# Kernel optimization log

Hardware: AMD Instinct MI355X
Metric: run time of the kernel (lower is better)

Reference implementation:

```python
import jax, jax.numpy as jnp
import numpy as np
from jax import lax

NH = 8  # heads


def _ln(x, g, b):
    m = x.mean(-1, keepdims=True)
    v = ((x - m) ** 2).mean(-1, keepdims=True)
    return (x - m) * lax.rsqrt(v + 1e-5) * g + b


def _pos_idx(n):
    # torch: linspace(n-1,0,n)[:,None] + linspace(0,n-1,n)[None,:], flattened long
    r = np.linspace(n - 1, 0, n).reshape(n, 1)
    c = np.linspace(0, n - 1, n).reshape(1, n)
    return jnp.asarray((r + c).reshape(-1).astype(np.int32))


def _mha(q_in, k_in, v_in, in_w, in_b, out_w, out_b, pos_enc=None, pos_idx=None, attn_mask=None):
    # MultiheadAttentionRelative: q/k/v proj + relative pos-encoding gather terms
    w, bsz, e = q_in.shape
    hd = e // NH
    scale = hd ** -0.5
    q = (q_in @ in_w[:e].T + in_b[:e]) * scale
    k = k_in @ in_w[e:2 * e].T + in_b[e:2 * e]
    v = v_in @ in_w[2 * e:].T + in_b[2 * e:]
    q = q.reshape(w, bsz, NH, hd)
    k = k.reshape(w, bsz, NH, hd)
    v = v.reshape(w, bsz, NH, hd)
    attn = jnp.einsum('wnec,vnec->newv', q, k)  # [N,E,W,W']
    if pos_enc is not None:
        pe = pos_enc[pos_idx].reshape(w, w, e)  # [2W-1,C] -> [W,W',C] gather
        q_r = ((pe @ in_w[:e].T + in_b[:e]) * scale).reshape(w, w, NH, hd)
        k_r = (pe @ in_w[e:2 * e].T + in_b[e:2 * e]).reshape(w, w, NH, hd)
        attn = attn + jnp.einsum('wnec,wvec->newv', q, k_r) + jnp.einsum('vnec,wvec->newv', k, q_r)
    if attn_mask is not None:
        attn = attn + attn_mask[None, None]
    raw = attn
    p = jax.nn.softmax(attn, axis=-1)
    v_o = jnp.einsum('newv,vnec->wnec', p, v).reshape(w, bsz, e)
    return v_o @ out_w.T + out_b, raw.sum(axis=1)


def _interp_lin(x, out_size):
    # torch F.interpolate(mode='linear', align_corners=False) along last axis
    L_in = x.shape[-1]
    if L_in == out_size:
        return x
    coords = jnp.clip((jnp.arange(out_size, dtype=jnp.float32) + 0.5) * (L_in / out_size) - 0.5, 0.0, L_in - 1.0)
    lo = jnp.floor(coords).astype(jnp.int32)
    hi = jnp.minimum(lo + 1, L_in - 1)
    frac = coords - lo.astype(jnp.float32)
    return x[..., lo] * (1.0 - frac) + x[..., hi] * frac


def _conv(x, w, b, pad):
    y = lax.conv_general_dilated(x, w, (1, 1), pad, dimension_numbers=('NCHW', 'OIHW', 'NCHW'))
    return y + b[None, :, None, None]


def _self_layer(feat, feat1, pos, pidx, pos1, pidx1, posy, pidxy, posy1, pidxy1, p):
    iw, ib, ow, ob, n1g, n1b, n2g, n2b = p
    f2 = _ln(feat, n1g, n1b)
    f4 = _ln(feat1, n2g, n2b)
    w_, h2, c = f2.shape
    w1_, h4, c1 = f4.shape
    # row<->col switch: [W,2HN,C] -> [HN,2W,C]
    f2y = jnp.transpose(f2.reshape(w_, 2, h2 // 2, c), (2, 1, 0, 3)).reshape(h2 // 2, 2 * w_, c)
    f4y = jnp.transpose(f4.reshape(w1_, 2, h4 // 2, c1), (2, 1, 0, 3)).reshape(h4 // 2, 2 * w1_, c1)
    f2y, _ = _mha(f2y, f2y, f2y, iw[1], ib[1], ow[1], ob[1], posy, pidxy)
    f2 = jnp.transpose(f2y.reshape(h2 // 2, 2, w_, c), (2, 1, 0, 3)).reshape(w_, h2, c)
    f4y, _ = _mha(f4y, f4y, f4y, iw[3], ib[3], ow[3], ob[3], posy1, pidxy1)
    f4 = jnp.transpose(f4y.reshape(h4 // 2, 2, w1_, c1), (2, 1, 0, 3)).reshape(w1_, h4, c1)
    f2, _ = _mha(f2, f2, f2, iw[0], ib[0], ow[0], ob[0], pos, pidx)
    f4, _ = _mha(f4, f4, f4, iw[2], ib[2], ow[2], ob[2], pos1, pidx1)
    return feat + f2, feat1 + f4


def _cross_layer(fl, fr, fl1, fr1, pos, pidx, pos1, pidx1, p, last):
    iw, ib, ow, ob, n1g, n1b, n2g, n2b, mw1, mb1, mw2, mb2 = p
    fl2 = _ln(fl, n1g, n1b)
    fr2 = _ln(fr, n1g, n1b)
    fl4 = _ln(fl1, n2g, n2b)
    fr4 = _ln(fr1, n2g, n2b)
    up_r, _ = _mha(fr2, fl2, fl2, iw[0], ib[0], ow[0], ob[0], jnp.flip(pos, 0), pidx)
    up_r1, _ = _mha(fr4, fl4, fl4, iw[1], ib[1], ow[1], ob[1], jnp.flip(pos1, 0), pidx1)
    fr = fr + up_r
    fr1n = fr1 + up_r1
    if last:
        w = fl2.shape[0]
        w1 = fl4.shape[0]
        m = jnp.where(jnp.triu(jnp.ones((w, w), jnp.float32), 1) == 1.0, -jnp.inf, 0.0)
        m1 = jnp.where(jnp.triu(jnp.ones((w1, w1), jnp.float32), 1) == 1.0, -jnp.inf, 0.0)
    else:
        m = None
        m1 = None
    fr2n = _ln(fr, n1g, n1b)
    up_l, raw = _mha(fl2, fr2n, fr2n, iw[0], ib[0], ow[0], ob[0], pos, pidx, m)
    fr4n = _ln(fr1n, n2g, n2b)
    up_l1, _ = _mha(fl4, fr4n, fr4n, iw[1], ib[1], ow[1], ob[1], pos1, pidx1, m1)
    fl = fl + up_l
    fl1n = fl1 + up_l1
    feat = jnp.concatenate([fl, fr], 1)        # [W,2HN,C]
    feat_n = jnp.concatenate([fl1n, fr1n], 1)  # [W1,2HN,C]
    x = jnp.transpose(feat_n, (2, 1, 0))       # [C,2HN,W1]
    x = _interp_lin(x, feat.shape[0])          # [C,2HN,W]
    feat_n = jnp.transpose(x, (2, 1, 0))
    feat_n = jnp.concatenate([feat_n, feat], 2)  # [W,2HN,2C]
    x = jnp.transpose(feat_n, (2, 1, 0))[None]   # [1,2C,2HN,W]
    x = _conv(x, mw1, mb1, 'VALID')
    x = _conv(x, mw2, mb2, ((1, 1), (1, 1)))
    out = jnp.transpose(x[0], (2, 1, 0))         # [W,2HN,C]
    return out, raw


def reference(feat_left, feat_right, feat_left1, feat_right1, pos_enc, pos_enc1, pos_enc_y, pos_enc_y1,
              sa_in_w, sa_in_b, sa_out_w, sa_out_b, sa_n1_g, sa_n1_b, sa_n2_g, sa_n2_b,
              ca_in_w, ca_in_b, ca_out_w, ca_out_b, ca_n1_g, ca_n1_b, ca_n2_g, ca_n2_b,
              merge_w1, merge_b1, merge_w2, merge_b2):
    bs, c, h, w = feat_left.shape
    w1 = feat_left1.shape[3]
    hn = h * bs

    def flat(x):
        return jnp.transpose(x, (3, 2, 0, 1)).reshape(x.shape[3], -1, c)  # [W,HN,C]

    fl, fr = flat(feat_left), flat(feat_right)
    fl1, fr1 = flat(feat_left1), flat(feat_right1)
    pidx = _pos_idx(w)
    pidx1 = _pos_idx(w1)
    pidxy = _pos_idx(hn)
    pidxy1 = _pos_idx(hn)
    feat = jnp.concatenate([fl, fr], 1)    # [W,2HN,C]
    feat1 = jnp.concatenate([fl1, fr1], 1)  # [W1,2HN,C]
    L = sa_in_w.shape[0]
    raw = None
    for i in range(L):
        sp = (sa_in_w[i], sa_in_b[i], sa_out_w[i], sa_out_b[i], sa_n1_g[i], sa_n1_b[i], sa_n2_g[i], sa_n2_b[i])
        feat, feat1 = _self_layer(feat, feat1, pos_enc, pidx, pos_enc1, pidx1, pos_enc_y, pidxy, pos_enc_y1, pidxy1, sp)
        cp = (ca_in_w[i], ca_in_b[i], ca_out_w[i], ca_out_b[i], ca_n1_g[i], ca_n1_b[i], ca_n2_g[i], ca_n2_b[i],
              merge_w1[i], merge_b1[i], merge_w2[i], merge_b2[i])
        feat, raw = _cross_layer(feat[:, :hn], feat[:, hn:], feat1[:, :hn], feat1[:, hn:],
                                 pos_enc, pidx, pos_enc1, pidx1, cp, i == L - 1)
    attn_weight = jnp.transpose(raw.reshape(h, bs, w, w), (1, 0, 2, 3))  # [N,H,W,W]
    return attn_weight


def setup_inputs() -> dict:
    key = jax.random.key(0)
    ks = iter(jax.random.split(key, 40))
    N, C, H, W, W1, Lyr = 1, 128, 64, 128, 64, 6
    s = 0.05
    d = {}
    d['feat_left'] = jax.random.normal(next(ks), (N, C, H, W), jnp.float32)
    d['feat_right'] = jax.random.normal(next(ks), (N, C, H, W), jnp.float32)
    d['feat_left1'] = jax.random.normal(next(ks), (N, C, H, W1), jnp.float32)
    d['feat_right1'] = jax.random.normal(next(ks), (N, C, H, W1), jnp.float32)
    d['pos_enc'] = jax.random.normal(next(ks), (2 * W - 1, C), jnp.float32) * 0.1
    d['pos_enc1'] = jax.random.normal(next(ks), (2 * W1 - 1, C), jnp.float32) * 0.1
    d['pos_enc_y'] = jax.random.normal(next(ks), (2 * H - 1, C), jnp.float32) * 0.1
    d['pos_enc_y1'] = jax.random.normal(next(ks), (2 * H - 1, C), jnp.float32) * 0.1
    d['sa_in_w'] = jax.random.normal(next(ks), (Lyr, 4, 3 * C, C), jnp.float32) * s
    d['sa_in_b'] = jnp.zeros((Lyr, 4, 3 * C), jnp.float32)
    d['sa_out_w'] = jax.random.normal(next(ks), (Lyr, 4, C, C), jnp.float32) * s
    d['sa_out_b'] = jnp.zeros((Lyr, 4, C), jnp.float32)
    d['sa_n1_g'] = jnp.ones((Lyr, C), jnp.float32)
    d['sa_n1_b'] = jnp.zeros((Lyr, C), jnp.float32)
    d['sa_n2_g'] = jnp.ones((Lyr, C), jnp.float32)
    d['sa_n2_b'] = jnp.zeros((Lyr, C), jnp.float32)
    d['ca_in_w'] = jax.random.normal(next(ks), (Lyr, 2, 3 * C, C), jnp.float32) * s
    d['ca_in_b'] = jnp.zeros((Lyr, 2, 3 * C), jnp.float32)
    d['ca_out_w'] = jax.random.normal(next(ks), (Lyr, 2, C, C), jnp.float32) * s
    d['ca_out_b'] = jnp.zeros((Lyr, 2, C), jnp.float32)
    d['ca_n1_g'] = jnp.ones((Lyr, C), jnp.float32)
    d['ca_n1_b'] = jnp.zeros((Lyr, C), jnp.float32)
    d['ca_n2_g'] = jnp.ones((Lyr, C), jnp.float32)
    d['ca_n2_b'] = jnp.zeros((Lyr, C), jnp.float32)
    d['merge_w1'] = jax.random.normal(next(ks), (Lyr, 128, 256, 1, 1), jnp.float32) * s
    d['merge_b1'] = jnp.zeros((Lyr, 128), jnp.float32)
    d['merge_w2'] = jax.random.normal(next(ks), (Lyr, 128, 128, 3, 3), jnp.float32) * s
    d['merge_b2'] = jnp.zeros((Lyr, 128), jnp.float32)
    return d
```

## Files before the change

### kernel.cpp

```cpp
#include <hip/hip_runtime.h>
#include <hip/hip_bf16.h>
#include <math.h>


typedef __attribute__((ext_vector_type(8))) short bf16x8;
typedef __attribute__((ext_vector_type(4))) float f32x4;
typedef __hip_bfloat16 bf16;

__device__ __forceinline__ float b2f(unsigned short u) {
  return __uint_as_float((unsigned)u << 16);
}
__device__ __forceinline__ short f2bs(float x) {
  bf16 h = __float2bfloat16(x);
  short s;
  __builtin_memcpy(&s, &h, 2);
  return s;
}
__device__ __forceinline__ int ymap(int t, int D0, int D1) {
  return (t % D0) * (2 * D1) + ((t / D0) & 1) * D1 + t / (2 * D0);
}


__global__ void k_build_feat(const float* __restrict__ L, const float* __restrict__ R,
                             float* __restrict__ feat, int W) {
  int t = blockIdx.x;
  int c = threadIdx.x;
  int b = t & 127;
  int w = t >> 7;
  const float* src = (b < 64) ? L : R;
  int h = b & 63;
  feat[(size_t)t * 128 + c] = src[((size_t)c * 64 + h) * W + w];
}

struct FDesc { const float* s; bf16* d; int n; };
struct FArgs { FDesc d[9]; int cum[10]; int nprob; };
__global__ void k_f2b_multi(FArgs fa) {
  int bid = blockIdx.x;
  int p = 0;
  while (p + 1 < fa.nprob && bid >= fa.cum[p + 1]) ++p;
  const FDesc d = fa.d[p];
  int i = (bid - fa.cum[p]) * 1024 + threadIdx.x * 4;
  if (i + 3 < d.n) {
    float4 x = *(const float4*)(d.s + i);
    d.d[i + 0] = __float2bfloat16(x.x);
    d.d[i + 1] = __float2bfloat16(x.y);
    d.d[i + 2] = __float2bfloat16(x.z);
    d.d[i + 3] = __float2bfloat16(x.w);
  } else {
    for (int z = 0; z < 4 && i + z < d.n; ++z) d.d[i + z] = __float2bfloat16(d.s[i + z]);
  }
}

__global__ void k_wfullb(const float* __restrict__ w2, bf16* __restrict__ wf) {
  int bid = blockIdx.x;
  int l = bid >> 7, co = bid & 127;
  int ci = threadIdx.x;
  const float* src = w2 + (size_t)l * 128 * 128 * 9;
  bf16* dst = wf + (size_t)l * 128 * 1152;
#pragma unroll
  for (int ky = 0; ky < 3; ky++)
#pragma unroll
    for (int kx = 0; kx < 3; kx++)
      dst[(size_t)co * 1152 + (kx * 3 + ky) * 128 + ci] =
          __float2bfloat16(src[((size_t)(co * 128 + ci) * 3 + ky) * 3 + kx]);
}

__global__ void k_zero_guard(bf16* p0, bf16* p1) {
  int t = threadIdx.x;
  p0[255 * 256 + t] = __float2bfloat16(0.0f);
  p1[127 * 256 + t] = __float2bfloat16(0.0f);
}

struct WCArgs { const bf16* iw[12]; const bf16* ow[12]; bf16* out[12]; };
__global__ __launch_bounds__(256) void k_wcomb(WCArgs a) {
  __shared__ bf16 sOw[128 * 128];
  int p = blockIdx.x / 6, rc = blockIdx.x % 6;
  const bf16* iw = a.iw[p];
  const bf16* ow = a.ow[p];
  for (int i = threadIdx.x; i < 128 * 16; i += 256)
    ((bf16x8*)sOw)[i] = ((const bf16x8*)ow)[i];
  __syncthreads();
  int row = rc * 64 + (threadIdx.x >> 2);
  int seg = (threadIdx.x & 3) * 32;
  float acc[32];
#pragma unroll
  for (int c = 0; c < 32; ++c) acc[c] = 0.f;
  for (int t = 0; t < 128; ++t) {
    float av = b2f((unsigned short)iw[row * 128 + t]);
#pragma unroll
    for (int c = 0; c < 32; ++c)
      acc[c] = fmaf(av, b2f((unsigned short)sOw[t * 128 + seg + c]), acc[c]);
  }
  bf16* o = a.out[p] + (size_t)row * 128 + seg;
  for (int c = 0; c < 32; ++c) o[c] = __float2bfloat16(acc[c]);
}

struct BCArgs { const float* iwf[12]; const float* obf[12]; const float* ibf[12]; float* out[12]; };
__global__ void k_bcomb(BCArgs a) {
  int p = blockIdx.x, j = threadIdx.x;
  const float* iw = a.iwf[p] + (size_t)j * 128;
  const float* ob = a.obf[p];
  float acc = a.ibf[p][j];
  for (int t = 0; t < 128; ++t) acc = fmaf(iw[t], ob[t], acc);
  a.out[p][j] = acc;
}

__global__ void k_rawcomb4(const float* __restrict__ A, const float* __restrict__ B2,
                           const float* __restrict__ C3, const float* __restrict__ D4,
                           bf16* __restrict__ out) {
  int i = blockIdx.x * 256 + threadIdx.x;
  int v = i & 127, w = (i >> 7) & 127;
  float rv = (v > w) ? 0.0f : (A[i] + B2[i] + C3[i] + D4[i]);
  out[i] = __float2bfloat16(rv);
}


struct LDesc { const float* src; bf16* dst; const float* g; const float* be;
               int ntok, Bout, PBin, offIn; };
struct LArgs { LDesc d[4]; int cum[5]; int nprob; };

__global__ __launch_bounds__(256) void k_ln_multi(LArgs la) {
  int bid = blockIdx.x;
  int p = 0;
  while (p + 1 < la.nprob && bid >= la.cum[p + 1]) ++p;
  const LDesc d = la.d[p];
  int t = (bid - la.cum[p]) * 4 + (threadIdx.x >> 6);
  int lane = threadIdx.x & 63;
  if (t >= d.ntok) return;
  int w = t / d.Bout, b = t - w * d.Bout;
  const float* row = d.src + (size_t)(w * d.PBin + d.offIn + b) * 128;
  float x0 = row[lane], x1 = row[lane + 64];
  float s = x0 + x1;
#pragma unroll
  for (int o = 32; o; o >>= 1) s += __shfl_xor(s, o, 64);
  float m = s * (1.0f / 128.0f);
  float d0 = x0 - m, d1 = x1 - m;
  float v = d0 * d0 + d1 * d1;
#pragma unroll
  for (int o = 32; o; o >>= 1) v += __shfl_xor(v, o, 64);
  float r = 1.0f / sqrtf(v * (1.0f / 128.0f) + 1e-5f);
  bf16* orow = d.dst + (size_t)t * 128;
  orow[lane]      = __float2bfloat16(d0 * r * d.g[lane]      + d.be[lane]);
  orow[lane + 64] = __float2bfloat16(d1 * r * d.g[lane + 64] + d.be[lane + 64]);
}


struct GDesc {
  const bf16* A; const float* Af0; const float* Af1;
  const bf16* W; const float* bias;
  bf16* Cb; float* Cf; const float* resid;
  int M, N, K, lda, scaleN;
  int imode, iD0, iD1;
  int omode, oD0, oD1, ooff;
};
struct GArgs { GDesc d[6]; int cum[7]; int nprob; };

__global__ __launch_bounds__(256) void k_gemm_multi(GArgs ga) {
  __shared__ bf16x8 sA[64 * 4];
  __shared__ bf16x8 sB[64 * 4];
  int bid = blockIdx.x;
  int p = 0;
  while (p + 1 < ga.nprob && bid >= ga.cum[p + 1]) ++p;
  const GDesc d = ga.d[p];
  int local = bid - ga.cum[p];
  int tilesx = d.N >> 6;
  int ty = local / tilesx, tx = local - ty * tilesx;
  const int m0 = ty << 6, n0 = tx << 6;
  const int tid = threadIdx.x;
  const int lane = tid & 63;
  const int wave = tid >> 6;
  const int wm = wave >> 1, wn = wave & 1;
  const int fr = lane & 15;
  const int kc = lane >> 4;
  f32x4 acc[2][2];
#pragma unroll
  for (int f = 0; f < 2; f++)
#pragma unroll
    for (int g = 0; g < 2; g++) acc[f][g] = (f32x4){0.f, 0.f, 0.f, 0.f};

  for (int k0 = 0; k0 < d.K; k0 += 32) {
    {
      int row = tid >> 2, ch = tid & 3;
      int m = m0 + row;
      bf16x8 val = (bf16x8){0, 0, 0, 0, 0, 0, 0, 0};
      if (d.imode == 0) {
        if (m < d.M) val = *(const bf16x8*)(d.A + (size_t)m * d.lda + k0 + ch * 8);
      } else if (d.imode == 1) {
        if (m < d.M) {
          int ar = ymap(m, d.iD0, d.iD1);
          val = *(const bf16x8*)(d.A + (size_t)ar * d.lda + k0 + ch * 8);
        }
      } else if (d.imode == 2) {
        int kblk = k0 >> 7;
        int kx = kblk / 3, ky = kblk - kx * 3;
        int arow = m + (kx - 1) * 128;
        int y = (m & 127) + (ky - 1);
        if (arow >= 0 && arow < d.M && y >= 0 && y < 128)
          val = *(const bf16x8*)(d.A + (size_t)arow * d.lda + (k0 & 127) + ch * 8);
      } else {
        int kk = k0 + ch * 8;
        int w = m >> 7, y = m & 127;
        if (kk < 128) {
          float xo = fminf(fmaxf(w * 0.5f - 0.25f, 0.0f), 63.0f);
          int lo = (int)xo;
          int hi = (lo + 1 < 63) ? lo + 1 : 63;
          float f = xo - (float)lo;
          const float* a0 = d.Af0 + ((size_t)lo * 128 + y) * 128 + kk;
          const float* a1 = d.Af0 + ((size_t)hi * 128 + y) * 128 + kk;
#pragma unroll
          for (int z = 0; z < 8; ++z) val[z] = f2bs(a0[z] * (1.0f - f) + a1[z] * f);
        } else {
          const float* a0 = d.Af1 + (size_t)m * 128 + (kk - 128);
#pragma unroll
          for (int z = 0; z < 8; ++z) val[z] = f2bs(a0[z]);
        }
      }
      sA[row * 4 + (ch ^ ((row >> 2) & 3))] = val;
      bf16x8 bval = *(const bf16x8*)(d.W + (size_t)(n0 + row) * d.K + k0 + ch * 8);
      sB[row * 4 + (ch ^ ((row >> 2) & 3))] = bval;
    }
    __syncthreads();
    bf16x8 af[2], bg[2];
#pragma unroll
    for (int f = 0; f < 2; ++f) {
      int row = wm * 32 + f * 16 + fr;
      af[f] = sA[row * 4 + (kc ^ ((row >> 2) & 3))];
    }
#pragma unroll
    for (int g = 0; g < 2; ++g) {
      int row = wn * 32 + g * 16 + fr;
      bg[g] = sB[row * 4 + (kc ^ ((row >> 2) & 3))];
    }
#pragma unroll
    for (int f = 0; f < 2; ++f)
#pragma unroll
      for (int g = 0; g < 2; ++g)
        acc[f][g] = __builtin_amdgcn_mfma_f32_16x16x32_bf16(af[f], bg[g], acc[f][g], 0, 0, 0);
    __syncthreads();
  }
  const int r4 = (lane >> 4) << 2;
  const int ocol = lane & 15;
#pragma unroll
  for (int f = 0; f < 2; ++f) {
#pragma unroll
    for (int g = 0; g < 2; ++g) {
      int n = n0 + wn * 32 + g * 16 + ocol;
      float bv = d.bias ? d.bias[n] : 0.0f;
      bool sc = (n < d.scaleN);
#pragma unroll
      for (int i = 0; i < 4; ++i) {
        int m = m0 + wm * 32 + f * 16 + r4 + i;
        if (m < d.M) {
          int row;
          if (d.omode == 0) row = (m / d.oD0) * d.oD1 + d.ooff + (m % d.oD0);
          else row = ymap(m, d.oD0, d.oD1);
          size_t idx = (size_t)row * d.N + n;
          float val = acc[f][g][i] + bv;
          if (sc) val *= 0.25f;
          if (d.resid) val += d.resid[idx];
          if (d.Cb) d.Cb[idx] = __float2bfloat16(val);
          else d.Cf[idx] = val;
        }
      }
    }
  }
}


struct ADesc {
  const bf16* Q; const bf16* K; const bf16* V;
  const bf16* PPb; bf16* O;
  float* raw0; float* raw1; float* raw2; float* raw3;
  int ldQ, ldK, ldV, Wlen, B, sflip, useMask;
};
struct AArgs { ADesc d[2]; int cum[3]; int nprob; };

template<int WLEN, int SGN>
__device__ __forceinline__ void attn_core(const ADesc& d, int b, int st, int h,
                                          int tid, bf16* Vt, bf16* Pl, bf16* T2l,
                                          bf16* Ost) {
  constexpr int NT = WLEN / 16;
  constexpr int R = WLEN - 1;
  const f32x4 z4 = (f32x4){0.f, 0.f, 0.f, 0.f};
  const bf16x8 zb = (bf16x8){0, 0, 0, 0, 0, 0, 0, 0};

  {
    int q = tid & (WLEN / 2 - 1);
    int cc = tid >> ((WLEN == 128) ? 6 : 5);
    constexpr int CH = (WLEN == 128) ? 16 : 8;
    int cb = cc * CH;
    const bf16* v0p = d.V + ((size_t)(2 * q) * d.B + b) * d.ldV + h * 64 + cb;
    const bf16* v1p = d.V + ((size_t)(2 * q + 1) * d.B + b) * d.ldV + h * 64 + cb;
#pragma unroll
    for (int j = 0; j < CH; j += 8) {
      bf16x8 a = *(const bf16x8*)(v0p + j);
      bf16x8 bb = *(const bf16x8*)(v1p + j);
#pragma unroll
      for (int z = 0; z < 8; ++z) {
        unsigned pk = (unsigned)(unsigned short)a[z] |
                      ((unsigned)(unsigned short)bb[z] << 16);
        *(unsigned*)(Vt + (size_t)(cb + j + z) * 136 + 2 * q) = pk;
      }
    }
  }
  __syncthreads();

  const int wave = tid >> 6, l = tid & 63;
  const int lm = l & 15, lg = l >> 4;
  const bool zlane = (lg >= 2);
  bf16* Pw  = Pl + wave * (16 * 136);
  bf16* T2w = T2l + wave * (16 * 20);
  int p0[4], src[4], hi[4], tsel[4];
  bool csel[4];
#pragma unroll
  for (int i = 0; i < 4; ++i) {
    p0[i] = SGN * (lm - 4 * lg - i) + 15;
    src[i] = (l & 48) | (p0[i] & 15);
    hi[i] = p0[i] & 16;
    if (SGN == 1) {
      int t0 = lm + 15 - 4 * lg - i;
      csel[i] = (t0 < 16);
      tsel[i] = csel[i] ? t0 : t0 - 16;
    } else {
      int t0 = lm - 15 + 4 * lg + i;
      csel[i] = (t0 >= 0);
      tsel[i] = csel[i] ? t0 : t0 + 16;
    }
  }

  const int w0 = st * 16;
  const int chb = h * 64 + wave * 16 + lg * 8;

  bf16x8 qf = zb;
  if (!zlane) qf = *(const bf16x8*)(d.Q + ((size_t)(w0 + lm) * d.B + b) * d.ldQ + chb);

  const int U0 = (SGN == 1) ? (R - w0 - 15) : (R + w0 - WLEN + 1);
  const int Ub0 = (SGN == 1) ? (R - w0 - 15) : (R - (WLEN - 16) + w0 - 15);
  const bf16* t1p = d.PPb + (size_t)(U0 + lm) * 256 + 128 + chb;
  const bf16* t2p = d.PPb + (size_t)(Ub0 + lm) * 256 + chb;
  const int v0i = ((SGN == 1) ? 0 : (WLEN - 16)) + lm;
  const bf16* kp = d.K + ((size_t)v0i * d.B + b) * d.ldK + chb;
  const ptrdiff_t kstep = (ptrdiff_t)SGN * 16 * d.B * d.ldK;

  f32x4 t1a;
  {
    bf16x8 z = zb;
    if (!zlane) z = *(const bf16x8*)t1p;
    t1p += 16 * 256;
    t1a = __builtin_amdgcn_mfma_f32_16x16x32_bf16(qf, z, z4, 0, 0, 0);
  }
  int v = v0i;
#pragma unroll
  for (int j = 0; j < NT; ++j) {
    f32x4 t1b;
    {
      bf16x8 z = zb;
      if (!zlane) z = *(const bf16x8*)t1p;
      t1p += 16 * 256;
      t1b = __builtin_amdgcn_mfma_f32_16x16x32_bf16(qf, z, z4, 0, 0, 0);
    }
    bf16x8 kf = zb;
    if (!zlane) kf = *(const bf16x8*)kp;
    kp += kstep;
    f32x4 s4 = __builtin_amdgcn_mfma_f32_16x16x32_bf16(qf, kf, z4, 0, 0, 0);
    bf16x8 zA = zb, zB = zb;
    if (!zlane) {
      zA = *(const bf16x8*)t2p;
      zB = *(const bf16x8*)(t2p + 16 * 256);
    }
    t2p += 16 * 256;
    f32x4 t2A = __builtin_amdgcn_mfma_f32_16x16x32_bf16(zA, kf, z4, 0, 0, 0);
    f32x4 t2B = __builtin_amdgcn_mfma_f32_16x16x32_bf16(zB, kf, z4, 0, 0, 0);
#pragma unroll
    for (int i = 0; i < 4; ++i)
      T2w[lm * 20 + tsel[i]] = f2bs(csel[i] ? t2A[i] : t2B[i]);
    ushort4 t2u = *(const ushort4*)(T2w + lm * 20 + 4 * lg);
    unsigned short t2a[4] = {t2u.x, t2u.y, t2u.z, t2u.w};
#pragma unroll
    for (int i = 0; i < 4; ++i) {
      float va = __shfl(t1a[i], src[i], 64);
      float vb = __shfl(t1b[i], src[i], 64);
      float s = s4[i] + (hi[i] ? vb : va) + b2f(t2a[i]);
      Pw[(4 * lg + i) * 136 + v] = f2bs(__expf(s));
    }
    t1a = t1b;
    v += SGN * 16;
  }
  const bf16x8 ones = (bf16x8){0x3F80, 0x3F80, 0x3F80, 0x3F80,
                               0x3F80, 0x3F80, 0x3F80, 0x3F80};
  f32x4 oa = z4, rsm = z4;
#pragma unroll
  for (int vc = 0; vc < NT / 2; ++vc) {
    bf16x8 pf = *(const bf16x8*)(Pw + lm * 136 + vc * 32 + lg * 8);
    bf16x8 vf = *(const bf16x8*)(Vt + (size_t)(wave * 16 + lm) * 136 + vc * 32 + lg * 8);
    oa = __builtin_amdgcn_mfma_f32_16x16x32_bf16(pf, vf, oa, 0, 0, 0);
    rsm = __builtin_amdgcn_mfma_f32_16x16x32_bf16(pf, ones, rsm, 0, 0, 0);
  }
#pragma unroll
  for (int i = 0; i < 4; ++i)
    Ost[(4 * lg + i) * 80 + wave * 16 + lm] = f2bs(oa[i] / rsm[i]);
  __syncthreads();
  if (tid < 128) {
    int row = tid >> 3, ch8 = (tid & 7) * 8;
    bf16x8 vv = *(const bf16x8*)(Ost + row * 80 + ch8);
    *(bf16x8*)(d.O + ((size_t)(w0 + row) * d.B + b) * 128 + h * 64 + ch8) = vv;
  }
}

__global__ __launch_bounds__(256, 4) void k_attn_mfma(AArgs aa) {
  __shared__ bf16 Vt[64 * 136];
  __shared__ bf16 Pl[4 * 16 * 136];
  __shared__ bf16 T2l[4 * 16 * 20];
  __shared__ bf16 Ost[16 * 80];
  int bid = blockIdx.x;
  int p = 0;
  while (p + 1 < aa.nprob && bid >= aa.cum[p + 1]) ++p;
  const ADesc d = aa.d[p];
  int local = bid - aa.cum[p];
  int b = local % d.B;
  int rest = local / d.B;
  int ns = d.Wlen >> 4;
  int st = rest % ns, h = rest / ns;
  int tid = threadIdx.x;
  if (d.Wlen == 128) {
    if (d.sflip == 1) attn_core<128, 1>(d, b, st, h, tid, Vt, Pl, T2l, Ost);
    else attn_core<128, -1>(d, b, st, h, tid, Vt, Pl, T2l, Ost);
  } else {
    if (d.sflip == 1) attn_core<64, 1>(d, b, st, h, tid, Vt, Pl, T2l, Ost);
    else attn_core<64, -1>(d, b, st, h, tid, Vt, Pl, T2l, Ost);
  }
}

__global__ __launch_bounds__(256, 2) void k_attn_raw(ADesc d) {
  __shared__ bf16 T2l[4 * 16 * 20];
  constexpr int NT = 8;
  constexpr int R = 127;
  const f32x4 z4 = (f32x4){0.f, 0.f, 0.f, 0.f};
  const bf16x8 zb = (bf16x8){0, 0, 0, 0, 0, 0, 0, 0};
  int bid = blockIdx.x;
  int b = bid % d.B, st = bid / d.B;
  int tid = threadIdx.x;
  const int wave = tid >> 6, l = tid & 63;
  const int lm = l & 15, lg = l >> 4;
  const bool zlane = (lg >= 2);
  bf16* T2w = T2l + wave * (16 * 20);
  int p0[4];
#pragma unroll
  for (int i = 0; i < 4; ++i) p0[i] = (lm - 4 * lg - i) + 15;
  const int w0 = st * 16;
  f32x4 raw[NT];
#pragma unroll
  for (int vt = 0; vt < NT; ++vt) raw[vt] = z4;

  for (int hh = 0; hh < 2; ++hh) {
    const int e = wave * 2 + hh;
    const int chb = e * 16 + lg * 8;
    bf16x8 qf = zb;
    if (!zlane) qf = *(const bf16x8*)(d.Q + ((size_t)(w0 + lm) * d.B + b) * d.ldQ + chb);
    const int U0 = R - w0 - 15;
    f32x4 t1a;
    {
      int u = min(max(U0 + lm, 0), 2 * R);
      bf16x8 z = zb;
      if (!zlane) z = *(const bf16x8*)(d.PPb + (size_t)u * 256 + 128 + chb);
      t1a = __builtin_amdgcn_mfma_f32_16x16x32_bf16(qf, z, z4, 0, 0, 0);
    }
#pragma unroll
    for (int j = 0; j < NT; ++j) {
      const int vt = j;
      const int v = vt * 16 + lm;
      f32x4 t1b;
      {
        int u = min(max(U0 + (j + 1) * 16 + lm, 0), 2 * R);
        bf16x8 z = zb;
        if (!zlane) z = *(const bf16x8*)(d.PPb + (size_t)u * 256 + 128 + chb);
        t1b = __builtin_amdgcn_mfma_f32_16x16x32_bf16(qf, z, z4, 0, 0, 0);
      }
      bf16x8 kf = zb;
      if (!zlane) kf = *(const bf16x8*)(d.K + ((size_t)v * d.B + b) * d.ldK + chb);
      f32x4 s4 = __builtin_amdgcn_mfma_f32_16x16x32_bf16(qf, kf, z4, 0, 0, 0);
      const int Ub = R + vt * 16 - w0 - 15;
#pragma unroll
      for (int u2 = 0; u2 < 2; ++u2) {
        int ua = min(max(Ub + u2 * 16 + lm, 0), 2 * R);
        bf16x8 z = zb;
        if (!zlane) z = *(const bf16x8*)(d.PPb + (size_t)ua * 256 + chb);
        f32x4 t2 = __builtin_amdgcn_mfma_f32_16x16x32_bf16(z, kf, z4, 0, 0, 0);
#pragma unroll
        for (int i = 0; i < 4; ++i) {
          int u = Ub + u2 * 16 + 4 * lg + i;
          int t = R + v - u - w0;
          if (t >= 0 && t < 16) T2w[lm * 20 + t] = f2bs(t2[i]);
        }
      }
      ushort4 t2u = *(const ushort4*)(T2w + lm * 20 + 4 * lg);
      unsigned short t2a[4] = {t2u.x, t2u.y, t2u.z, t2u.w};
#pragma unroll
      for (int i = 0; i < 4; ++i) {
        int src = (l & 48) | (p0[i] & 15);
        float va = __shfl(t1a[i], src, 64);
        float vb = __shfl(t1b[i], src, 64);
        float s = s4[i] + ((p0[i] & 16) ? vb : va) + b2f(t2a[i]);
        if (v > (w0 + 4 * lg + i)) s = -INFINITY;
        raw[vt][i] += s;
      }
      t1a = t1b;
    }
  }
  float* rp = (wave == 0) ? d.raw0 : (wave == 1) ? d.raw1 : (wave == 2) ? d.raw2 : d.raw3;
#pragma unroll
  for (int vt = 0; vt < NT; ++vt)
#pragma unroll
    for (int i = 0; i < 4; ++i)
      rp[((size_t)b * 128 + (w0 + 4 * lg + i)) * 128 + vt * 16 + lm] = raw[vt][i];
}


extern "C" void kernel_launch(void* const* d_in, const int* in_sizes, int n_in,
                              void* d_out, int out_size, void* d_ws, size_t ws_size,
                              hipStream_t stream) {
  (void)in_sizes; (void)n_in; (void)out_size; (void)ws_size;
  const float* FLt  = (const float*)d_in[0];
  const float* FRt  = (const float*)d_in[1];
  const float* FL1t = (const float*)d_in[2];
  const float* FR1t = (const float*)d_in[3];
  const float* PE   = (const float*)d_in[4];
  const float* PE1  = (const float*)d_in[5];
  const float* PEY  = (const float*)d_in[6];
  const float* PEY1 = (const float*)d_in[7];
  const float* SA_IW = (const float*)d_in[8];
  const float* SA_IB = (const float*)d_in[9];
  const float* SA_OW = (const float*)d_in[10];
  const float* SA_OB = (const float*)d_in[11];
  const float* SA_N1G = (const float*)d_in[12];
  const float* SA_N1B = (const float*)d_in[13];
  const float* SA_N2G = (const float*)d_in[14];
  const float* SA_N2B = (const float*)d_in[15];
  const float* CA_IW = (const float*)d_in[16];
  const float* CA_IB = (const float*)d_in[17];
  const float* CA_OW = (const float*)d_in[18];
  const float* CA_OB = (const float*)d_in[19];
  const float* CA_N1G = (const float*)d_in[20];
  const float* CA_N1B = (const float*)d_in[21];
  const float* CA_N2G = (const float*)d_in[22];
  const float* CA_N2B = (const float*)d_in[23];
  const float* MW1 = (const float*)d_in[24];
  const float* MB1 = (const float*)d_in[25];
  const float* MW2 = (const float*)d_in[26];
  const float* MB2 = (const float*)d_in[27];

  float* ws = (float*)d_ws;
  float* FEAT  = ws;
  float* FEAT1 = ws + 2097152;
  float* FN2   = ws + 3145728;
  bf16* PP0b   = (bf16*)(ws + 4194304);
  bf16* PP1b   = (bf16*)(ws + 4259840);
  float* B2f   = ws + 4276224;
  bf16* hb = (bf16*)(ws + 4292608);
  bf16* QKV   = hb;
  bf16* QKV1  = hb + 6291456;
  bf16* Xb    = hb + 9437184;
  bf16* XBb   = hb + 11534336;
  bf16* Ob    = hb + 12582912;
  bf16* Ob1   = hb + 14680064;
  bf16* PEb   = hb + 15728640;
  bf16* PE1b  = hb + 15761408;
  bf16* PEYb  = hb + 15777792;
  bf16* PEY1b = hb + 15794176;
  bf16* SAIWb = hb + 15810560;
  bf16* SAOWb = hb + 18169856;
  bf16* CAIWb = hb + 18563072;
  bf16* CAOWb = hb + 19742720;
  bf16* MW1b  = hb + 19939328;
  bf16* WFb   = hb + 20135936;
  bf16* W2b   = hb + 21020672;

  bf16* QR   = QKV + 3145728;
  bf16* FL4F = QKV + 4194304;
  bf16* QR1  = QKV + 5767168;
  bf16* KVq  = QKV1;
  bf16* KVq1 = QKV1 + 2097152;
  bf16* XR2  = Xb;
  bf16* XR21 = Xb + 1048576;

  GArgs ga; int ng = 0; int gb = 0;
  auto gadd = [&](GDesc gd) { ga.cum[ng] = gb; ga.d[ng] = gd;
                              gb += ((gd.M + 63) >> 6) * (gd.N >> 6); ++ng; };
  auto gflush = [&]() { ga.nprob = ng;
                        k_gemm_multi<<<gb, 256, 0, stream>>>(ga); ng = 0; gb = 0; };
  LArgs la; int nl = 0; int lb = 0;
  auto lnadd = [&](LDesc ld) { la.cum[nl] = lb; la.d[nl] = ld;
                               lb += (ld.ntok + 3) / 4; ++nl; };
  auto lnflush = [&]() { la.nprob = nl;
                         k_ln_multi<<<lb, 256, 0, stream>>>(la); nl = 0; lb = 0; };
  AArgs aa; int na = 0; int ab = 0;
  auto aadd = [&](ADesc ad) { aa.cum[na] = ab; aa.d[na] = ad;
                              ab += ad.B * (ad.Wlen >> 4) * 2; ++na; };
  auto aflush = [&]() { aa.nprob = na;
                        k_attn_mfma<<<ab, 256, 0, stream>>>(aa); na = 0; ab = 0; };

  auto G = [&](const bf16* A, const bf16* W, const float* bias,
               bf16* Cb, float* Cf, const float* resid,
               int M, int N, int K, int lda, int scaleN,
               int imode, int iD0, int iD1,
               int omode, int oD0, int oD1, int ooff,
               const float* Af0 = nullptr, const float* Af1 = nullptr) {
    GDesc gd; gd.A = A; gd.Af0 = Af0; gd.Af1 = Af1; gd.W = W; gd.bias = bias;
    gd.Cb = Cb; gd.Cf = Cf; gd.resid = resid;
    gd.M = M; gd.N = N; gd.K = K; gd.lda = lda; gd.scaleN = scaleN;
    gd.imode = imode; gd.iD0 = iD0; gd.iD1 = iD1;
    gd.omode = omode; gd.oD0 = oD0; gd.oD1 = oD1; gd.ooff = ooff;
    gadd(gd);
  };
  auto AT = [&](const bf16* Q, int ldQ, const bf16* K, int ldK, const bf16* V, int ldV,
                const bf16* PPb, int Wlen, int B, int sflip, bf16* O) {
    ADesc ad; ad.Q = Q; ad.K = K; ad.V = V; ad.PPb = PPb; ad.O = O;
    ad.raw0 = nullptr; ad.raw1 = nullptr; ad.raw2 = nullptr; ad.raw3 = nullptr;
    ad.ldQ = ldQ; ad.ldK = ldK; ad.ldV = ldV; ad.Wlen = Wlen; ad.B = B;
    ad.sflip = sflip; ad.useMask = 0;
    aadd(ad);
  };

  {
    FArgs fa; int nf = 0; int fb = 0;
    auto fadd = [&](const float* s, bf16* dd, int n) {
      fa.cum[nf] = fb; fa.d[nf] = FDesc{s, dd, n}; fb += (n + 1023) / 1024; ++nf; };
    fadd(SA_IW, SAIWb, 6 * 4 * 384 * 128);
    fadd(SA_OW, SAOWb, 6 * 4 * 128 * 128);
    fadd(CA_IW, CAIWb, 6 * 2 * 384 * 128);
    fadd(CA_OW, CAOWb, 6 * 2 * 128 * 128);
    fadd(MW1,   MW1b,  6 * 128 * 256);
    fadd(PE,    PEb,   255 * 128);
    fadd(PE1,   PE1b,  127 * 128);
    fadd(PEY,   PEYb,  127 * 128);
    fadd(PEY1,  PEY1b, 127 * 128);
    fa.nprob = nf;
    k_f2b_multi<<<fb, 256, 0, stream>>>(fa);
  }
  k_wfullb<<<768, 128, 0, stream>>>(MW2, WFb);
  k_zero_guard<<<1, 256, 0, stream>>>(PP0b, PP1b);
  {
    WCArgs wc; BCArgs bc;
    for (int l = 0; l < 6; ++l) {
      for (int s = 0; s < 2; ++s) {
        int p = l * 2 + s;
        int iwi = (s == 0) ? 0 : 2;
        int owi = (s == 0) ? 1 : 3;
        wc.iw[p]  = SAIWb + (size_t)l * 4 * 384 * 128 + (size_t)iwi * 384 * 128;
        wc.ow[p]  = SAOWb + (size_t)l * 4 * 128 * 128 + (size_t)owi * 128 * 128;
        wc.out[p] = W2b + (size_t)p * 384 * 128;
        bc.iwf[p] = SA_IW + (size_t)l * 4 * 384 * 128 + (size_t)iwi * 384 * 128;
        bc.obf[p] = SA_OB + (size_t)l * 4 * 128 + (size_t)owi * 128;
        bc.ibf[p] = SA_IB + (size_t)l * 4 * 384 + (size_t)iwi * 384;
        bc.out[p] = B2f + (size_t)p * 384;
      }
    }
    k_wcomb<<<72, 256, 0, stream>>>(wc);
    k_bcomb<<<12, 384, 0, stream>>>(bc);
  }
  k_build_feat<<<16384, 128, 0, stream>>>(FLt, FRt, FEAT, 128);
  k_build_feat<<<8192, 128, 0, stream>>>(FL1t, FR1t, FEAT1, 64);

  for (int l = 0; l < 6; ++l) {
    bool last = (l == 5);
    const bf16* iw  = SAIWb + (size_t)l * 4 * 384 * 128;
    const float* ib = SA_IB + (size_t)l * 4 * 384;
    const bf16* ow  = SAOWb + (size_t)l * 4 * 128 * 128;
    const float* ob = SA_OB + (size_t)l * 4 * 128;
    const bf16* ciw  = CAIWb + (size_t)l * 2 * 384 * 128;
    const float* cib = CA_IB + (size_t)l * 2 * 384;
    const bf16* cow  = CAOWb + (size_t)l * 2 * 128 * 128;
    const float* cob = CA_OB + (size_t)l * 2 * 128;
    const bf16* ciw1 = ciw + 384 * 128;
    const float* cib1 = cib + 384;
    const bf16* cow1 = cow + 128 * 128;
    const float* cob1 = cob + 128;
    const int IW = 384 * 128, OW = 128 * 128;

    lnadd(LDesc{FEAT, Xb, SA_N1G + l * 128, SA_N1B + l * 128, 16384, 128, 128, 0});
    if (!last) lnadd(LDesc{FEAT1, XBb, SA_N2G + l * 128, SA_N2B + l * 128, 8192, 128, 128, 0});
    lnflush();
    G(Xb, iw + IW, ib + 384, QKV, nullptr, nullptr, 16384, 384, 128, 128, 128, 1, 128, 64, 0, 1, 1, 0);
    if (!last) G(XBb, iw + 3 * IW, ib + 3 * 384, QKV1, nullptr, nullptr, 8192, 384, 128, 128, 128, 1, 64, 64, 0, 1, 1, 0);
    G(PEYb, iw + IW, ib + 384, PP0b, nullptr, nullptr, 127, 256, 128, 128, 128, 0, 0, 0, 0, 1, 1, 0);
    if (!last) G(PEY1b, iw + 3 * IW, ib + 3 * 384, PP1b, nullptr, nullptr, 127, 256, 128, 128, 128, 0, 0, 0, 0, 1, 1, 0);
    gflush();
    AT(QKV, 384, QKV + 128, 384, QKV + 256, 384, PP0b, 64, 256, 1, Ob);
    if (!last) AT(QKV1, 384, QKV1 + 128, 384, QKV1 + 256, 384, PP1b, 64, 128, 1, Ob1);
    aflush();
    G(Ob, W2b + (size_t)(l * 2) * 49152, B2f + (l * 2) * 384, QKV, nullptr, nullptr,
      16384, 384, 128, 128, 128, 1, 64, 128, 0, 1, 1, 0);
    if (!last) G(Ob1, W2b + (size_t)(l * 2 + 1) * 49152, B2f + (l * 2 + 1) * 384, QKV1,
                 nullptr, nullptr, 8192, 384, 128, 128, 128, 1, 64, 64, 0, 1, 1, 0);
    G(PEb, iw, ib, PP0b, nullptr, nullptr, 255, 256, 128, 128, 128, 0, 0, 0, 0, 1, 1, 0);
    if (!last) G(PE1b, iw + 2 * IW, ib + 2 * 384, PP1b, nullptr, nullptr, 127, 256, 128, 128, 128, 0, 0, 0, 0, 1, 1, 0);
    gflush();
    AT(QKV, 384, QKV + 128, 384, QKV + 256, 384, PP0b, 128, 128, 1, Ob);
    if (!last) AT(QKV1, 384, QKV1 + 128, 384, QKV1 + 256, 384, PP1b, 64, 128, 1, Ob1);
    aflush();
    G(Ob, ow, ob, nullptr, FEAT, FEAT, 16384, 128, 128, 128, 0, 0, 0, 0, 0, 1, 1, 0);
    if (!last) G(Ob1, ow + 2 * OW, ob + 2 * 128, nullptr, FEAT1, FEAT1, 8192, 128, 128, 128, 0, 0, 0, 0, 0, 1, 1, 0);
    gflush();

    lnadd(LDesc{FEAT, Xb, CA_N1G + l * 128, CA_N1B + l * 128, 8192, 64, 128, 0});
    lnadd(LDesc{FEAT, Xb + 1048576, CA_N1G + l * 128, CA_N1B + l * 128, 8192, 64, 128, 64});
    if (!last) {
      lnadd(LDesc{FEAT1, XBb, CA_N2G + l * 128, CA_N2B + l * 128, 4096, 64, 128, 0});
      lnadd(LDesc{FEAT1, XBb + 524288, CA_N2G + l * 128, CA_N2B + l * 128, 4096, 64, 128, 64});
    }
    lnflush();
    G(Xb, ciw, cib, QKV, nullptr, nullptr, 8192, 384, 128, 128, 128, 0, 0, 0, 0, 1, 1, 0);
    G(Xb + 1048576, ciw, cib, QR, nullptr, nullptr, 8192, 128, 128, 128, 128, 0, 0, 0, 0, 1, 1, 0);
    if (!last) {
      G(XBb, ciw1, cib1, FL4F, nullptr, nullptr, 4096, 384, 128, 128, 128, 0, 0, 0, 0, 1, 1, 0);
      G(XBb + 524288, ciw1, cib1, QR1, nullptr, nullptr, 4096, 128, 128, 128, 128, 0, 0, 0, 0, 1, 1, 0);
    }
    G(PEb, ciw, cib, PP0b, nullptr, nullptr, 255, 256, 128, 128, 128, 0, 0, 0, 0, 1, 1, 0);
    if (!last) G(PE1b, ciw1, cib1, PP1b, nullptr, nullptr, 127, 256, 128, 128, 128, 0, 0, 0, 0, 1, 1, 0);
    gflush();
    AT(QR, 128, QKV + 128, 384, QKV + 256, 384, PP0b, 128, 64, -1, Ob);
    if (!last) AT(QR1, 128, FL4F + 128, 384, FL4F + 256, 384, PP1b, 64, 64, -1, Ob1);
    aflush();
    G(Ob, cow, cob, nullptr, FEAT, FEAT, 8192, 128, 128, 128, 0, 0, 0, 0, 0, 64, 128, 64);
    if (!last) G(Ob1, cow1, cob1, nullptr, FN2, FEAT1, 4096, 128, 128, 128, 0, 0, 0, 0, 0, 64, 128, 64);
    gflush();
    lnadd(LDesc{FEAT, XR2, CA_N1G + l * 128, CA_N1B + l * 128, 8192, 64, 128, 64});
    if (!last) lnadd(LDesc{FN2, XR21, CA_N2G + l * 128, CA_N2B + l * 128, 4096, 64, 128, 64});
    lnflush();
    G(XR2, ciw + 128 * 128, cib + 128, KVq, nullptr, nullptr, 8192, 256, 128, 128, 0, 0, 0, 0, 0, 1, 1, 0);
    if (!last) G(XR21, ciw1 + 128 * 128, cib1 + 128, KVq1, nullptr, nullptr, 4096, 256, 128, 128, 0, 0, 0, 0, 0, 1, 1, 0);
    gflush();
    if (last) {
      ADesc ad; ad.Q = QKV; ad.K = KVq; ad.V = KVq + 128; ad.PPb = PP0b;
      ad.O = nullptr;
      ad.raw0 = FEAT1; ad.raw1 = FN2; ad.raw2 = (float*)Ob; ad.raw3 = (float*)FL4F;
      ad.ldQ = 384; ad.ldK = 256; ad.ldV = 256;
      ad.Wlen = 128; ad.B = 64; ad.sflip = 1; ad.useMask = 1;
      k_attn_raw<<<64 * 8, 256, 0, stream>>>(ad);
      k_rawcomb4<<<4096, 256, 0, stream>>>(FEAT1, FN2, (float*)Ob, (float*)FL4F,
                                           (bf16*)d_out);
      break;
    }
    AT(QKV, 384, KVq, 256, KVq + 128, 256, PP0b, 128, 64, 1, Ob);
    AT(FL4F, 384, KVq1, 256, KVq1 + 128, 256, PP1b, 64, 64, 1, Ob1);
    aflush();
    G(Ob, cow, cob, nullptr, FEAT, FEAT, 8192, 128, 128, 128, 0, 0, 0, 0, 0, 64, 128, 0);
    G(Ob1, cow1, cob1, nullptr, FN2, FEAT1, 4096, 128, 128, 128, 0, 0, 0, 0, 0, 64, 128, 0);
    gflush();
    G(nullptr, MW1b + (size_t)l * 128 * 256, MB1 + l * 128, Ob, nullptr, nullptr,
      16384, 128, 256, 256, 0, 3, 0, 0, 0, 1, 1, 0, FN2, FEAT);
    gflush();
    G(Ob, WFb + (size_t)l * 128 * 1152, MB2 + l * 128, nullptr, FEAT, nullptr,
      16384, 128, 1152, 128, 0, 2, 0, 0, 0, 1, 1, 0);
    gflush();
  }
}
```

Baseline: 1.617 ms.

## Fuse raw-attention head sum into attention kernel; size attention smem dynamically

The final raw-attention kernel no longer writes four per-wave fp32 partial maps to global memory for a separate combine kernel. It stages them in a 32KB shared buffer, sums them, applies the causal zero mask and writes bf16 output directly. Separately, k_attn_mfma now uses dynamic shared memory sized to the largest window in the batch, so 64-wide problems use a narrower row stride. The extra shared memory in k_attn_raw may reduce its occupancy.

```diff
diff --git a/kernel.cpp b/kernel.cpp
--- a/kernel.cpp
+++ b/kernel.cpp
@@ -103,15 +103,6 @@
   float acc = a.ibf[p][j];
   for (int t = 0; t < 128; ++t) acc = fmaf(iw[t], ob[t], acc);
   a.out[p][j] = acc;
-}
-
-__global__ void k_rawcomb4(const float* __restrict__ A, const float* __restrict__ B2,
-                           const float* __restrict__ C3, const float* __restrict__ D4,
-                           bf16* __restrict__ out) {
-  int i = blockIdx.x * 256 + threadIdx.x;
-  int v = i & 127, w = (i >> 7) & 127;
-  float rv = (v > w) ? 0.0f : (A[i] + B2[i] + C3[i] + D4[i]);
-  out[i] = __float2bfloat16(rv);
 }
 
 
@@ -270,19 +261,22 @@
 struct ADesc {
   const bf16* Q; const bf16* K; const bf16* V;
   const bf16* PPb; bf16* O;
-  float* raw0; float* raw1; float* raw2; float* raw3;
   int ldQ, ldK, ldV, Wlen, B, sflip, useMask;
 };
 struct AArgs { ADesc d[2]; int cum[3]; int nprob; };
 
 template<int WLEN, int SGN>
 __device__ __forceinline__ void attn_core(const ADesc& d, int b, int st, int h,
-                                          int tid, bf16* Vt, bf16* Pl, bf16* T2l,
-                                          bf16* Ost) {
+                                          int tid, bf16* smem) {
   constexpr int NT = WLEN / 16;
   constexpr int R = WLEN - 1;
+  constexpr int PST = WLEN + 8;
   const f32x4 z4 = (f32x4){0.f, 0.f, 0.f, 0.f};
   const bf16x8 zb = (bf16x8){0, 0, 0, 0, 0, 0, 0, 0};
+  bf16* Vt  = smem;
+  bf16* Pl  = smem + 64 * PST;
+  bf16* T2l = smem + 128 * PST;
+  bf16* Ost = T2l + 1280;
 
   {
     int q = tid & (WLEN / 2 - 1);
@@ -299,7 +293,7 @@
       for (int z = 0; z < 8; ++z) {
         unsigned pk = (unsigned)(unsigned short)a[z] |
                       ((unsigned)(unsigned short)bb[z] << 16);
-        *(unsigned*)(Vt + (size_t)(cb + j + z) * 136 + 2 * q) = pk;
+        *(unsigned*)(Vt + (size_t)(cb + j + z) * PST + 2 * q) = pk;
       }
     }
   }
@@ -308,7 +302,7 @@
   const int wave = tid >> 6, l = tid & 63;
   const int lm = l & 15, lg = l >> 4;
   const bool zlane = (lg >= 2);
-  bf16* Pw  = Pl + wave * (16 * 136);
+  bf16* Pw  = Pl + wave * (16 * PST);
   bf16* T2w = T2l + wave * (16 * 20);
   int p0[4], src[4], hi[4], tsel[4];
   bool csel[4];
@@ -381,7 +375,7 @@
       float va = __shfl(t1a[i], src[i], 64);
       float vb = __shfl(t1b[i], src[i], 64);
       float s = s4[i] + (hi[i] ? vb : va) + b2f(t2a[i]);
-      Pw[(4 * lg + i) * 136 + v] = f2bs(__expf(s));
+      Pw[(4 * lg + i) * PST + v] = f2bs(__expf(s));
     }
     t1a = t1b;
     v += SGN * 16;
@@ -391,8 +385,8 @@
   f32x4 oa = z4, rsm = z4;
 #pragma unroll
   for (int vc = 0; vc < NT / 2; ++vc) {
-    bf16x8 pf = *(const bf16x8*)(Pw + lm * 136 + vc * 32 + lg * 8);
-    bf16x8 vf = *(const bf16x8*)(Vt + (size_t)(wave * 16 + lm) * 136 + vc * 32 + lg * 8);
+    bf16x8 pf = *(const bf16x8*)(Pw + lm * PST + vc * 32 + lg * 8);
+    bf16x8 vf = *(const bf16x8*)(Vt + (size_t)(wave * 16 + lm) * PST + vc * 32 + lg * 8);
     oa = __builtin_amdgcn_mfma_f32_16x16x32_bf16(pf, vf, oa, 0, 0, 0);
     rsm = __builtin_amdgcn_mfma_f32_16x16x32_bf16(pf, ones, rsm, 0, 0, 0);
   }
@@ -408,10 +402,7 @@
 }
 
 __global__ __launch_bounds__(256, 4) void k_attn_mfma(AArgs aa) {
-  __shared__ bf16 Vt[64 * 136];
-  __shared__ bf16 Pl[4 * 16 * 136];
-  __shared__ bf16 T2l[4 * 16 * 20];
-  __shared__ bf16 Ost[16 * 80];
+  extern __shared__ bf16 smem[];
   int bid = blockIdx.x;
   int p = 0;
   while (p + 1 < aa.nprob && bid >= aa.cum[p + 1]) ++p;
@@ -423,16 +414,17 @@
   int st = rest % ns, h = rest / ns;
   int tid = threadIdx.x;
   if (d.Wlen == 128) {
-    if (d.sflip == 1) attn_core<128, 1>(d, b, st, h, tid, Vt, Pl, T2l, Ost);
-    else attn_core<128, -1>(d, b, st, h, tid, Vt, Pl, T2l, Ost);
+    if (d.sflip == 1) attn_core<128, 1>(d, b, st, h, tid, smem);
+    else attn_core<128, -1>(d, b, st, h, tid, smem);
   } else {
-    if (d.sflip == 1) attn_core<64, 1>(d, b, st, h, tid, Vt, Pl, T2l, Ost);
-    else attn_core<64, -1>(d, b, st, h, tid, Vt, Pl, T2l, Ost);
+    if (d.sflip == 1) attn_core<64, 1>(d, b, st, h, tid, smem);
+    else attn_core<64, -1>(d, b, st, h, tid, smem);
   }
 }
 
 __global__ __launch_bounds__(256, 2) void k_attn_raw(ADesc d) {
   __shared__ bf16 T2l[4 * 16 * 20];
+  __shared__ float Rl[4][16][128];
   constexpr int NT = 8;
   constexpr int R = 127;
   const f32x4 z4 = (f32x4){0.f, 0.f, 0.f, 0.f};
@@ -507,12 +499,23 @@
       t1a = t1b;
     }
   }
-  float* rp = (wave == 0) ? d.raw0 : (wave == 1) ? d.raw1 : (wave == 2) ? d.raw2 : d.raw3;
 #pragma unroll
   for (int vt = 0; vt < NT; ++vt)
 #pragma unroll
     for (int i = 0; i < 4; ++i)
-      rp[((size_t)b * 128 + (w0 + 4 * lg + i)) * 128 + vt * 16 + lm] = raw[vt][i];
+      Rl[wave][4 * lg + i][vt * 16 + lm] = raw[vt][i];
+  __syncthreads();
+  {
+    int r = tid >> 4, v8 = (tid & 15) * 8;
+    int w = w0 + r;
+    bf16* out = d.O + ((size_t)b * 128 + w) * 128;
+#pragma unroll
+    for (int z = 0; z < 8; ++z) {
+      int vv = v8 + z;
+      float sum = Rl[0][r][vv] + Rl[1][r][vv] + Rl[2][r][vv] + Rl[3][r][vv];
+      out[vv] = __float2bfloat16((vv > w) ? 0.0f : sum);
+    }
+  }
 }
 
 
@@ -593,11 +596,14 @@
                                lb += (ld.ntok + 3) / 4; ++nl; };
   auto lnflush = [&]() { la.nprob = nl;
                          k_ln_multi<<<lb, 256, 0, stream>>>(la); nl = 0; lb = 0; };
-  AArgs aa; int na = 0; int ab = 0;
+  AArgs aa; int na = 0; int ab = 0; int maxw = 0;
   auto aadd = [&](ADesc ad) { aa.cum[na] = ab; aa.d[na] = ad;
-                              ab += ad.B * (ad.Wlen >> 4) * 2; ++na; };
+                              ab += ad.B * (ad.Wlen >> 4) * 2;
+                              if (ad.Wlen > maxw) maxw = ad.Wlen; ++na; };
   auto aflush = [&]() { aa.nprob = na;
-                        k_attn_mfma<<<ab, 256, 0, stream>>>(aa); na = 0; ab = 0; };
+                        size_t sh = (size_t)(128 * (maxw + 8) + 2560) * 2;
+                        k_attn_mfma<<<ab, 256, sh, stream>>>(aa);
+                        na = 0; ab = 0; maxw = 0; };
 
   auto G = [&](const bf16* A, const bf16* W, const float* bias,
                bf16* Cb, float* Cf, const float* resid,
@@ -615,7 +621,6 @@
   auto AT = [&](const bf16* Q, int ldQ, const bf16* K, int ldK, const bf16* V, int ldV,
                 const bf16* PPb, int Wlen, int B, int sflip, bf16* O) {
     ADesc ad; ad.Q = Q; ad.K = K; ad.V = V; ad.PPb = PPb; ad.O = O;
-    ad.raw0 = nullptr; ad.raw1 = nullptr; ad.raw2 = nullptr; ad.raw3 = nullptr;
     ad.ldQ = ldQ; ad.ldK = ldK; ad.ldV = ldV; ad.Wlen = Wlen; ad.B = B;
     ad.sflip = sflip; ad.useMask = 0;
     aadd(ad);
@@ -732,13 +737,10 @@
     gflush();
     if (last) {
       ADesc ad; ad.Q = QKV; ad.K = KVq; ad.V = KVq + 128; ad.PPb = PP0b;
-      ad.O = nullptr;
-      ad.raw0 = FEAT1; ad.raw1 = FN2; ad.raw2 = (float*)Ob; ad.raw3 = (float*)FL4F;
+      ad.O = (bf16*)d_out;
       ad.ldQ = 384; ad.ldK = 256; ad.ldV = 256;
       ad.Wlen = 128; ad.B = 64; ad.sflip = 1; ad.useMask = 1;
       k_attn_raw<<<64 * 8, 256, 0, stream>>>(ad);
-      k_rawcomb4<<<4096, 256, 0, stream>>>(FEAT1, FN2, (float*)Ob, (float*)FL4F,
-                                           (bf16*)d_out);
       break;
     }
     AT(QKV, 384, KVq, 256, KVq + 128, 256, PP0b, 128, 64, 1, Ob);
```

Result: no change. 1.593 ms (-1.5%).
